# Optimization experiments

Hardware: AMD Instinct MI355X
Metric: run time of the kernel (lower is better)

The kernel has to match this reference:

```python
import math
import jax, jax.numpy as jnp
import numpy as np

B, N, C = 2, 2048, 1024
H = 16
D = C // H  # 64
LN_EPS = 1e-5


def setup_inputs() -> dict:
    key = jax.random.key(0)
    ks = jax.random.split(key, 5)
    x = jax.random.normal(ks[0], (B, N, C), dtype=jnp.float32)
    w_qkv = jax.random.normal(ks[1], (C, 3 * C), dtype=jnp.float32) * 0.02
    w_proj = jax.random.normal(ks[2], (C, C), dtype=jnp.float32) * 0.02
    b_proj = jnp.zeros((C,), dtype=jnp.float32)
    ln_w = jnp.ones((D,), dtype=jnp.float32) + jax.random.normal(ks[3], (D,), dtype=jnp.float32) * 0.02
    ln_b = jax.random.normal(ks[4], (D,), dtype=jnp.float32) * 0.02
    return {"x": x, "w_qkv": w_qkv, "w_proj": w_proj, "b_proj": b_proj,
            "ln_w": ln_w, "ln_b": ln_b}


def _layernorm(t, w, b):
    mu = jnp.mean(t, axis=-1, keepdims=True)
    var = jnp.var(t, axis=-1, keepdims=True)
    return (t - mu) * jax.lax.rsqrt(var + LN_EPS) * w + b


def reference(x, w_qkv, w_proj, b_proj, ln_w, ln_b):
    b, n, c = x.shape
    h, d = H, c // H
    # QKV projection (no bias): [b,n,3c] -> [3,b,h,n,d]
    qkv = (x @ w_qkv).reshape(b, n, 3, h, d).transpose(2, 0, 3, 1, 4)
    q, k, v = qkv[0], qkv[1], qkv[2]
    # per-head LayerNorm on q and k (qk_norm)
    q = _layernorm(q, ln_w, ln_b)
    k = _layernorm(k, ln_w, ln_b)
    # NOTE: source multiplies q by sqrt(head_dim) (faithful to original)
    q = q * jnp.asarray(math.sqrt(d), dtype=q.dtype)
    scores = jnp.einsum('bhnd,bhmd->bhnm', q, k)  # [b,h,n,n]
    mask_value = -jnp.finfo(scores.dtype).max
    causal = jnp.tril(jnp.ones((n, n), dtype=bool))
    scores = jnp.where(causal, scores, mask_value)
    attn = jax.nn.softmax(scores, axis=-1)
    out = jnp.einsum('bhnm,bhmd->bhnd', attn, v)  # [b,h,n,d]
    out = out.transpose(0, 2, 1, 3).reshape(b, n, c)  # b n (h d)
    return out @ w_proj + b_proj
```

## Files before the change

kernel.cpp:

```cpp
#include <hip/hip_runtime.h>

#define LOG2E 1.4426950408889634f

typedef _Float16 f16x8_t __attribute__((ext_vector_type(8)));
typedef _Float16 f16x4_t __attribute__((ext_vector_type(4)));
typedef float    f32x4_t __attribute__((ext_vector_type(4)));

#define MFMA32(a, b, c) __builtin_amdgcn_mfma_f32_16x16x32_f16(a, b, c, 0, 0, 0)
#define MFMA16(a, b, c) __builtin_amdgcn_mfma_f32_16x16x16f16(a, b, c, 0, 0, 0)

__device__ __forceinline__ void async_copy16(void* lds, const void* g) {
    __builtin_amdgcn_global_load_lds(
        (const __attribute__((address_space(1))) unsigned char*)g,
        (__attribute__((address_space(3))) unsigned char*)lds, 16, 0, 0);
}

__global__ void cast_f32_f16_k(const float* __restrict__ in, _Float16* __restrict__ out, int n4) {
    int i = blockIdx.x * blockDim.x + threadIdx.x;
    if (i >= n4) return;
    float4 v = ((const float4*)in)[i];
    f16x4_t o = { (_Float16)v.x, (_Float16)v.y, (_Float16)v.z, (_Float16)v.w };
    ((f16x4_t*)out)[i] = o;
}

__global__ void transpose_cast_k(const float* __restrict__ in, _Float16* __restrict__ out,
                                 int R, int C) {
    __shared__ _Float16 tl[64][65];
    const int t = threadIdx.x;
    const int c = t & 63;
    const int r4 = t >> 6;
    const int r0 = blockIdx.y * 64, c0 = blockIdx.x * 64;
#pragma unroll
    for (int i = 0; i < 16; ++i) {
        int r = r4 + i * 4;
        tl[c][r] = (_Float16)in[(size_t)(r0 + r) * C + c0 + c];
    }
    __syncthreads();
#pragma unroll
    for (int i = 0; i < 16; ++i) {
        int rr = r4 + i * 4;
        out[(size_t)(c0 + rr) * R + r0 + c] = tl[rr][c];
    }
}

__global__ void vtrans_k(const _Float16* __restrict__ qkv, _Float16* __restrict__ VTg) {
    __shared__ _Float16 tl[64][65];
    const int t = threadIdx.x;
    const int bh = blockIdx.x;
    const int b = bh >> 4, h = bh & 15;
    const int n0 = blockIdx.y * 64;
    const int c = t & 63;
    const int r4 = t >> 6;
#pragma unroll
    for (int i = 0; i < 16; ++i) {
        int r = r4 + i * 4;
        tl[c][r] = qkv[(size_t)(b * 2048 + n0 + r) * 3072 + 2048 + h * 64 + c];
    }
    __syncthreads();
#pragma unroll
    for (int i = 0; i < 16; ++i) {
        int d = r4 + i * 4;
        VTg[(size_t)bh * 131072 + (size_t)d * 2048 + n0 + c] = tl[d][c];
    }
}

template <typename OutT, bool BIAS>
__global__ __launch_bounds__(256, 2)
void gemm_f16_k(const _Float16* __restrict__ A, const _Float16* __restrict__ BT,
                OutT* __restrict__ C, const float* __restrict__ bias,
                int M, int N, int K) {
    __shared__ _Float16 As[2][128][32];
    __shared__ _Float16 Bs[2][128][32];
    const int tid = threadIdx.x;
    const int wid = tid >> 6, lane = tid & 63;
    const int qd = lane >> 4, ln = lane & 15;
    const int m0 = blockIdx.x * 128, n0 = blockIdx.y * 128;
    const int wm = (wid >> 1) * 64, wn = (wid & 1) * 64;

    f32x4_t acc[4][4] = {};

    const int srow = lane >> 2;
    const int skk  = (lane & 3) * 8;

    for (int k0 = 0; k0 < K; k0 += 64) {
        __syncthreads();
#pragma unroll
        for (int p = 0; p < 4; ++p) {
            const int seg = p * 4 + wid;
            const int s   = seg >> 3;
            const int rg  = seg & 7;
            const int row = rg * 16 + srow;
            const size_t goff = (size_t)row * K + k0 + s * 32 + skk;
            async_copy16(&As[0][0][0] + seg * 512, A  + (size_t)m0 * K + goff);
            async_copy16(&Bs[0][0][0] + seg * 512, BT + (size_t)n0 * K + goff);
        }
        __syncthreads();
#pragma unroll
        for (int s = 0; s < 2; ++s) {
            f16x8_t a[4], b[4];
#pragma unroll
            for (int i = 0; i < 4; ++i)
                a[i] = *(const f16x8_t*)&As[s][wm + i * 16 + ln][qd * 8];
#pragma unroll
            for (int j = 0; j < 4; ++j)
                b[j] = *(const f16x8_t*)&Bs[s][wn + j * 16 + ln][qd * 8];
#pragma unroll
            for (int i = 0; i < 4; ++i)
#pragma unroll
                for (int j = 0; j < 4; ++j)
                    acc[i][j] = MFMA32(a[i], b[j], acc[i][j]);
        }
    }
#pragma unroll
    for (int i = 0; i < 4; ++i)
#pragma unroll
        for (int j = 0; j < 4; ++j) {
            const int col = n0 + wn + j * 16 + ln;
            const float bv = BIAS ? bias[col] : 0.0f;
#pragma unroll
            for (int r = 0; r < 4; ++r) {
                const int row = m0 + wm + i * 16 + qd * 4 + r;
                C[(size_t)row * N + col] = (OutT)(acc[i][j][r] + bv);
            }
        }
}

__global__ __launch_bounds__(256, 2)
void gemm_f16_m64_k(const _Float16* __restrict__ A, const _Float16* __restrict__ BT,
                    float* __restrict__ C, const float* __restrict__ bias,
                    int M, int N, int K) {
    __shared__ _Float16 As[2][64][32];
    __shared__ _Float16 Bs[2][128][32];
    const int tid = threadIdx.x;
    const int wid = tid >> 6, lane = tid & 63;
    const int qd = lane >> 4, ln = lane & 15;
    const int m0 = blockIdx.x * 64, n0 = blockIdx.y * 128;
    const int wn = wid * 32;

    f32x4_t acc[4][2] = {};
    const int srow = lane >> 2;
    const int skk  = (lane & 3) * 8;

    for (int k0 = 0; k0 < K; k0 += 64) {
        __syncthreads();
#pragma unroll
        for (int p = 0; p < 2; ++p) {
            const int seg = p * 4 + wid;
            const int hidx = seg * 512 + lane * 8;
            const int s_ = hidx >> 11;
            const int row = (hidx >> 5) & 63;
            const int kk = hidx & 31;
            async_copy16(&As[0][0][0] + seg * 512,
                         A + (size_t)(m0 + row) * K + k0 + s_ * 32 + kk);
        }
#pragma unroll
        for (int p = 0; p < 4; ++p) {
            const int seg = p * 4 + wid;
            const int s   = seg >> 3;
            const int rg  = seg & 7;
            const int row = rg * 16 + srow;
            async_copy16(&Bs[0][0][0] + seg * 512,
                         BT + (size_t)(n0 + row) * K + k0 + s * 32 + skk);
        }
        __syncthreads();
#pragma unroll
        for (int s = 0; s < 2; ++s) {
            f16x8_t a[4], b[2];
#pragma unroll
            for (int i = 0; i < 4; ++i)
                a[i] = *(const f16x8_t*)&As[s][i * 16 + ln][qd * 8];
#pragma unroll
            for (int j = 0; j < 2; ++j)
                b[j] = *(const f16x8_t*)&Bs[s][wn + j * 16 + ln][qd * 8];
#pragma unroll
            for (int i = 0; i < 4; ++i)
#pragma unroll
                for (int j = 0; j < 2; ++j)
                    acc[i][j] = MFMA32(a[i], b[j], acc[i][j]);
        }
    }
#pragma unroll
    for (int i = 0; i < 4; ++i)
#pragma unroll
        for (int j = 0; j < 2; ++j) {
            const int col = n0 + wn + j * 16 + ln;
            const float bv = bias[col];
#pragma unroll
            for (int r = 0; r < 4; ++r) {
                const int row = m0 + i * 16 + qd * 4 + r;
                C[(size_t)row * N + col] = acc[i][j][r] + bv;
            }
        }
}

__global__ void ln_qk_k(const _Float16* __restrict__ qkv, const float* __restrict__ ln_w,
                        const float* __restrict__ ln_b, _Float16* __restrict__ Qb,
                        _Float16* __restrict__ Kb) {
    const int tid = threadIdx.x;
    const int wid = tid >> 6, lane = tid & 63;
    const int row = blockIdx.x * 4 + wid;
    const int t = row >> 4;
    const int h = row & 15;
    const int b = t >> 11, n = t & 2047;
    const size_t base = (size_t)t * 3072 + h * 64 + lane;
    float q = (float)qkv[base];
    float k = (float)qkv[base + 1024];
    const float wv = ln_w[lane], bv = ln_b[lane];

    float sq = q, sk = k;
#pragma unroll
    for (int m = 1; m < 64; m <<= 1) { sq += __shfl_xor(sq, m); sk += __shfl_xor(sk, m); }
    sq *= (1.0f / 64.0f); sk *= (1.0f / 64.0f);
    const float dq = q - sq, dk = k - sk;
    float vq = dq * dq, vk = dk * dk;
#pragma unroll
    for (int m = 1; m < 64; m <<= 1) { vq += __shfl_xor(vq, m); vk += __shfl_xor(vk, m); }
    vq *= (1.0f / 64.0f); vk *= (1.0f / 64.0f);
    const float yq = dq * rsqrtf(vq + 1e-5f) * wv + bv;
    const float yk = dk * rsqrtf(vk + 1e-5f) * wv + bv;
    const size_t obase = ((size_t)((b * 16 + h) * 2048 + n)) * 64 + lane;
    Qb[obase] = (_Float16)(yq * (8.0f * LOG2E));
    Kb[obase] = (_Float16)yk;
}

__global__ __launch_bounds__(128, 3)
void attn_k(const _Float16* __restrict__ Q, const _Float16* __restrict__ K,
            const _Float16* __restrict__ VTg, _Float16* __restrict__ O) {
    __shared__ _Float16 Ks[2][64][32];
    __shared__ _Float16 VT[64][64];

    const int tid = threadIdx.x;
    const int wid = tid >> 6, lane = tid & 63;
    const int qd = lane >> 4, ln = lane & 15;
    const int bh = blockIdx.x;
    const int b = bh >> 4, h = bh & 15;
    const int pr = blockIdx.y >> 1;
    const int half = blockIdx.y & 1;
    const int hib = 31 - pr, lob = pr;
    const size_t kvbase = (size_t)bh * 2048 * 64;
    const size_t vtbase = (size_t)bh * 131072;
    const int qh0 = hib * 64 + half * 32 + wid * 16;
    const int ql0 = lob * 64 + half * 32 + wid * 16;

    f16x8_t qfh[2], qfl[2];
#pragma unroll
    for (int s = 0; s < 2; ++s) {
        qfh[s] = *(const f16x8_t*)&Q[kvbase + (size_t)(qh0 + ln) * 64 + s * 32 + qd * 8];
        qfl[s] = *(const f16x8_t*)&Q[kvbase + (size_t)(ql0 + ln) * 64 + s * 32 + qd * 8];
    }

    f32x4_t oh[4] = {}, olo[4] = {};
    float mh = -3.0e38f, ml = -3.0e38f;
    float lh = 0.0f, ll = 0.0f;

    const int vrow = (lane >> 3);
    const int vY   = (lane & 7) ^ (vrow & 7);

    const int nst = hib + 1;

    for (int st = 0; st < nst; ++st) {
        const int kv0 = st * 64;
        __syncthreads();
#pragma unroll
        for (int p = 0; p < 4; ++p) {
            const int seg = p * 2 + wid;
            const int oh_ = seg * 512;
            const int hidx = oh_ + lane * 8;
            const int s_ = hidx >> 11;
            const int rrow = (hidx >> 5) & 63;
            const int kk = hidx & 31;
            async_copy16((_Float16*)Ks + oh_,
                         K + kvbase + (size_t)(kv0 + rrow) * 64 + s_ * 32 + kk);
        }
#pragma unroll
        for (int p = 0; p < 4; ++p) {
            const int seg = p * 2 + wid;
            const int d = seg * 8 + vrow;
            async_copy16(&VT[0][0] + seg * 512,
                         VTg + vtbase + (size_t)d * 2048 + kv0 + vY * 8);
        }
        __syncthreads();

        f16x8_t kb[4][2];
#pragma unroll
        for (int jt = 0; jt < 4; ++jt)
#pragma unroll
            for (int s = 0; s < 2; ++s)
                kb[jt][s] = *(const f16x8_t*)&Ks[s][jt * 16 + ln][qd * 8];
        f16x4_t vf[4][4];
#pragma unroll
        for (int dt = 0; dt < 4; ++dt)
#pragma unroll
            for (int c = 0; c < 4; ++c)
                vf[dt][c] = *(const f16x4_t*)
                    &VT[dt * 16 + ln][(((2 * c + (qd >> 1)) ^ (ln & 7)) << 3) + (qd & 1) * 4];

        auto process = [&](const f16x8_t (&qf)[2], f32x4_t (&o)[4], float& m, float& l,
                           int q0w, bool diag) {
            f32x4_t sc[4];
#pragma unroll
            for (int jt = 0; jt < 4; ++jt) {
                f32x4_t s = {};
                s = MFMA32(kb[jt][0], qf[0], s);
                s = MFMA32(kb[jt][1], qf[1], s);
                sc[jt] = s;
            }
            if (diag) {
                const int qq = q0w + ln;
#pragma unroll
                for (int c = 0; c < 4; ++c)
#pragma unroll
                    for (int r = 0; r < 4; ++r)
                        if (kv0 + c * 16 + qd * 4 + r > qq) sc[c][r] = -3.0e38f;
            }
            float mx = sc[0][0];
#pragma unroll
            for (int c = 0; c < 4; ++c)
#pragma unroll
                for (int r = 0; r < 4; ++r) mx = fmaxf(mx, sc[c][r]);
            mx = fmaxf(mx, __shfl_xor(mx, 16));
            mx = fmaxf(mx, __shfl_xor(mx, 32));
            const float mn = fmaxf(m, mx);
            const float al = exp2f(m - mn);
            m = mn;
            float rs = 0.0f;
            f16x4_t pf[4];
#pragma unroll
            for (int c = 0; c < 4; ++c)
#pragma unroll
                for (int r = 0; r < 4; ++r) {
                    const float p = exp2f(sc[c][r] - mn);
                    rs += p;
                    pf[c][r] = (_Float16)p;
                }
            l = l * al + rs;
#pragma unroll
            for (int dt = 0; dt < 4; ++dt) o[dt] *= al;
#pragma unroll
            for (int dt = 0; dt < 4; ++dt)
#pragma unroll
                for (int c = 0; c < 4; ++c)
                    o[dt] = MFMA16(vf[dt][c], pf[c], o[dt]);
        };

        process(qfh, oh, mh, lh, qh0, st == hib);
        if (st <= lob) process(qfl, olo, ml, ll, ql0, st == lob);
    }

    auto epi = [&](f32x4_t (&o)[4], float l, int q0w) {
        float t = l + __shfl_xor(l, 16);
        t = t + __shfl_xor(t, 32);
        const float inv = 1.0f / t;
        const size_t base = ((size_t)(b * 2048 + q0w + ln)) * 1024 + h * 64 + qd * 4;
#pragma unroll
        for (int dt = 0; dt < 4; ++dt) {
            f16x4_t ov;
#pragma unroll
            for (int r = 0; r < 4; ++r) ov[r] = (_Float16)(o[dt][r] * inv);
            *(f16x4_t*)&O[base + dt * 16] = ov;
        }
    };
    epi(oh, lh, qh0);
    epi(olo, ll, ql0);
}

extern "C" void kernel_launch(void* const* d_in, const int* in_sizes, int n_in,
                              void* d_out, int out_size, void* d_ws, size_t ws_size,
                              hipStream_t stream) {
    const float* x      = (const float*)d_in[0];
    const float* w_qkv  = (const float*)d_in[1];
    const float* w_proj = (const float*)d_in[2];
    const float* b_proj = (const float*)d_in[3];
    const float* ln_w   = (const float*)d_in[4];
    const float* ln_b   = (const float*)d_in[5];
    float* out = (float*)d_out;

    char* w = (char*)d_ws;
    _Float16*  qkv    = (_Float16*)w;  w += (size_t)4096 * 3072 * 2;
    _Float16*  xh     = (_Float16*)w;  w += (size_t)4096 * 1024 * 2;
    _Float16*  wqkvT  = (_Float16*)w;  w += (size_t)3072 * 1024 * 2;
    _Float16*  wprojT = (_Float16*)w;  w += (size_t)1024 * 1024 * 2;
    _Float16*  Qb     = (_Float16*)w;  w += (size_t)32 * 2048 * 64 * 2;
    _Float16*  Kb     = (_Float16*)w;  w += (size_t)32 * 2048 * 64 * 2;
    _Float16*  VTg    = (_Float16*)w;  w += (size_t)32 * 64 * 2048 * 2;
    _Float16*  Ah     = (_Float16*)w;  w += (size_t)4096 * 1024 * 2;

    cast_f32_f16_k<<<4096, 256, 0, stream>>>(x, xh, 4096 * 1024 / 4);
    transpose_cast_k<<<dim3(48, 16), 256, 0, stream>>>(w_qkv, wqkvT, 1024, 3072);
    transpose_cast_k<<<dim3(16, 16), 256, 0, stream>>>(w_proj, wprojT, 1024, 1024);
    gemm_f16_k<_Float16, false><<<dim3(32, 24), 256, 0, stream>>>(xh, wqkvT, qkv, nullptr, 4096, 3072, 1024);
    vtrans_k<<<dim3(32, 32), 256, 0, stream>>>(qkv, VTg);
    ln_qk_k<<<16384, 256, 0, stream>>>(qkv, ln_w, ln_b, Qb, Kb);
    attn_k<<<dim3(32, 32), 128, 0, stream>>>(Qb, Kb, VTg, Ah);
    gemm_f16_m64_k<<<dim3(64, 8), 256, 0, stream>>>(Ah, wprojT, out, b_proj, 4096, 1024, 1024);
}
```

Measured before the change: 234.1 us.

## Split causal attention into KV chunks with double-buffered staging and merge pass

```diff
diff --git a/kernel.cpp b/kernel.cpp
--- a/kernel.cpp
+++ b/kernel.cpp
@@ -223,135 +223,134 @@
     Kb[obase] = (_Float16)yk;
 }
 
-__global__ __launch_bounds__(128, 3)
-void attn_k(const _Float16* __restrict__ Q, const _Float16* __restrict__ K,
-            const _Float16* __restrict__ VTg, _Float16* __restrict__ O) {
-    __shared__ _Float16 Ks[2][64][32];
-    __shared__ _Float16 VT[64][64];
+__global__ __launch_bounds__(256, 3)
+void attn_part_k(const _Float16* __restrict__ Q, const _Float16* __restrict__ K,
+                 const _Float16* __restrict__ VTg, _Float16* __restrict__ O,
+                 float* __restrict__ Op, float* __restrict__ ml) {
+    __shared__ _Float16 Ks[2][2][64][32];
+    __shared__ _Float16 VT[2][64][64];
 
     const int tid = threadIdx.x;
     const int wid = tid >> 6, lane = tid & 63;
     const int qd = lane >> 4, ln = lane & 15;
     const int bh = blockIdx.x;
     const int b = bh >> 4, h = bh & 15;
-    const int pr = blockIdx.y >> 1;
-    const int half = blockIdx.y & 1;
-    const int hib = 31 - pr, lob = pr;
+    const int y = blockIdx.y;
+    int band, chunk, nst;
+    if (y < 16)      { band = 16 + y; chunk = 0; nst = 16; }
+    else if (y < 32) { band = 47 - y; chunk = 1; nst = band - 15; }
+    else             { band = 47 - y; chunk = 0; nst = band + 1; }
     const size_t kvbase = (size_t)bh * 2048 * 64;
     const size_t vtbase = (size_t)bh * 131072;
-    const int qh0 = hib * 64 + half * 32 + wid * 16;
-    const int ql0 = lob * 64 + half * 32 + wid * 16;
-
-    f16x8_t qfh[2], qfl[2];
-#pragma unroll
-    for (int s = 0; s < 2; ++s) {
-        qfh[s] = *(const f16x8_t*)&Q[kvbase + (size_t)(qh0 + ln) * 64 + s * 32 + qd * 8];
-        qfl[s] = *(const f16x8_t*)&Q[kvbase + (size_t)(ql0 + ln) * 64 + s * 32 + qd * 8];
-    }
-
-    f32x4_t oh[4] = {}, olo[4] = {};
-    float mh = -3.0e38f, ml = -3.0e38f;
-    float lh = 0.0f, ll = 0.0f;
-
-    const int vrow = (lane >> 3);
+    const int qrow0 = band * 64 + wid * 16;
+    const int kvbeg = chunk * 1024;
+
+    f16x8_t qf[2];
+#pragma unroll
+    for (int s = 0; s < 2; ++s)
+        qf[s] = *(const f16x8_t*)&Q[kvbase + (size_t)(qrow0 + ln) * 64 + s * 32 + qd * 8];
+
+    f32x4_t o[4] = {};
+    float m = -3.0e38f, l = 0.0f;
+
+    const int vrow = lane >> 3;
     const int vY   = (lane & 7) ^ (vrow & 7);
-
-    const int nst = hib + 1;
-
-    for (int st = 0; st < nst; ++st) {
-        const int kv0 = st * 64;
-        __syncthreads();
-#pragma unroll
-        for (int p = 0; p < 4; ++p) {
-            const int seg = p * 2 + wid;
-            const int oh_ = seg * 512;
-            const int hidx = oh_ + lane * 8;
+    const int khidx_base = lane * 8;
+
+    auto stage = [&](int buf, int kv0) {
+#pragma unroll
+        for (int p = 0; p < 2; ++p) {
+            const int seg = p * 4 + wid;
+            const int hidx = seg * 512 + khidx_base;
             const int s_ = hidx >> 11;
             const int rrow = (hidx >> 5) & 63;
             const int kk = hidx & 31;
-            async_copy16((_Float16*)Ks + oh_,
+            async_copy16(&Ks[buf][0][0][0] + seg * 512,
                          K + kvbase + (size_t)(kv0 + rrow) * 64 + s_ * 32 + kk);
         }
 #pragma unroll
-        for (int p = 0; p < 4; ++p) {
-            const int seg = p * 2 + wid;
+        for (int p = 0; p < 2; ++p) {
+            const int seg = p * 4 + wid;
             const int d = seg * 8 + vrow;
-            async_copy16(&VT[0][0] + seg * 512,
+            async_copy16(&VT[buf][0][0] + seg * 512,
                          VTg + vtbase + (size_t)d * 2048 + kv0 + vY * 8);
         }
+    };
+
+    stage(0, kvbeg);
+
+    for (int st = 0; st < nst; ++st) {
+        const int kv0 = kvbeg + st * 64;
         __syncthreads();
+        if (st + 1 < nst) stage((st + 1) & 1, kv0 + 64);
+        const int buf = st & 1;
 
         f16x8_t kb[4][2];
 #pragma unroll
         for (int jt = 0; jt < 4; ++jt)
 #pragma unroll
             for (int s = 0; s < 2; ++s)
-                kb[jt][s] = *(const f16x8_t*)&Ks[s][jt * 16 + ln][qd * 8];
+                kb[jt][s] = *(const f16x8_t*)&Ks[buf][s][jt * 16 + ln][qd * 8];
         f16x4_t vf[4][4];
 #pragma unroll
         for (int dt = 0; dt < 4; ++dt)
 #pragma unroll
             for (int c = 0; c < 4; ++c)
                 vf[dt][c] = *(const f16x4_t*)
-                    &VT[dt * 16 + ln][(((2 * c + (qd >> 1)) ^ (ln & 7)) << 3) + (qd & 1) * 4];
-
-        auto process = [&](const f16x8_t (&qf)[2], f32x4_t (&o)[4], float& m, float& l,
-                           int q0w, bool diag) {
-            f32x4_t sc[4];
-#pragma unroll
-            for (int jt = 0; jt < 4; ++jt) {
-                f32x4_t s = {};
-                s = MFMA32(kb[jt][0], qf[0], s);
-                s = MFMA32(kb[jt][1], qf[1], s);
-                sc[jt] = s;
+                    &VT[buf][dt * 16 + ln][(((2 * c + (qd >> 1)) ^ (ln & 7)) << 3) + (qd & 1) * 4];
+
+        f32x4_t sc[4];
+#pragma unroll
+        for (int jt = 0; jt < 4; ++jt) {
+            f32x4_t s = {};
+            s = MFMA32(kb[jt][0], qf[0], s);
+            s = MFMA32(kb[jt][1], qf[1], s);
+            sc[jt] = s;
+        }
+        if (chunk * 16 + st == band) {
+            const int qq = qrow0 + ln;
+#pragma unroll
+            for (int c = 0; c < 4; ++c)
+#pragma unroll
+                for (int r = 0; r < 4; ++r)
+                    if (kv0 + c * 16 + qd * 4 + r > qq) sc[c][r] = -3.0e38f;
+        }
+        float mx = sc[0][0];
+#pragma unroll
+        for (int c = 0; c < 4; ++c)
+#pragma unroll
+            for (int r = 0; r < 4; ++r) mx = fmaxf(mx, sc[c][r]);
+        mx = fmaxf(mx, __shfl_xor(mx, 16));
+        mx = fmaxf(mx, __shfl_xor(mx, 32));
+        const float mn = fmaxf(m, mx);
+        const float al = exp2f(m - mn);
+        m = mn;
+        float rs = 0.0f;
+        f16x4_t pf[4];
+#pragma unroll
+        for (int c = 0; c < 4; ++c)
+#pragma unroll
+            for (int r = 0; r < 4; ++r) {
+                const float p = exp2f(sc[c][r] - mn);
+                rs += p;
+                pf[c][r] = (_Float16)p;
             }
-            if (diag) {
-                const int qq = q0w + ln;
-#pragma unroll
-                for (int c = 0; c < 4; ++c)
-#pragma unroll
-                    for (int r = 0; r < 4; ++r)
-                        if (kv0 + c * 16 + qd * 4 + r > qq) sc[c][r] = -3.0e38f;
-            }
-            float mx = sc[0][0];
+        l = l * al + rs;
+#pragma unroll
+        for (int dt = 0; dt < 4; ++dt) o[dt] *= al;
+#pragma unroll
+        for (int dt = 0; dt < 4; ++dt)
 #pragma unroll
             for (int c = 0; c < 4; ++c)
-#pragma unroll
-                for (int r = 0; r < 4; ++r) mx = fmaxf(mx, sc[c][r]);
-            mx = fmaxf(mx, __shfl_xor(mx, 16));
-            mx = fmaxf(mx, __shfl_xor(mx, 32));
-            const float mn = fmaxf(m, mx);
-            const float al = exp2f(m - mn);
-            m = mn;
-            float rs = 0.0f;
-            f16x4_t pf[4];
-#pragma unroll
-            for (int c = 0; c < 4; ++c)
-#pragma unroll
-                for (int r = 0; r < 4; ++r) {
-                    const float p = exp2f(sc[c][r] - mn);
-                    rs += p;
-                    pf[c][r] = (_Float16)p;
-                }
-            l = l * al + rs;
-#pragma unroll
-            for (int dt = 0; dt < 4; ++dt) o[dt] *= al;
-#pragma unroll
-            for (int dt = 0; dt < 4; ++dt)
-#pragma unroll
-                for (int c = 0; c < 4; ++c)
-                    o[dt] = MFMA16(vf[dt][c], pf[c], o[dt]);
-        };
-
-        process(qfh, oh, mh, lh, qh0, st == hib);
-        if (st <= lob) process(qfl, olo, ml, ll, ql0, st == lob);
-    }
-
-    auto epi = [&](f32x4_t (&o)[4], float l, int q0w) {
-        float t = l + __shfl_xor(l, 16);
-        t = t + __shfl_xor(t, 32);
-        const float inv = 1.0f / t;
-        const size_t base = ((size_t)(b * 2048 + q0w + ln)) * 1024 + h * 64 + qd * 4;
+                o[dt] = MFMA16(vf[dt][c], pf[c], o[dt]);
+    }
+
+    float lt = l + __shfl_xor(l, 16);
+    lt = lt + __shfl_xor(lt, 32);
+
+    if (band < 16) {
+        const float inv = 1.0f / lt;
+        const size_t base = ((size_t)(b * 2048 + qrow0 + ln)) * 1024 + h * 64 + qd * 4;
 #pragma unroll
         for (int dt = 0; dt < 4; ++dt) {
             f16x4_t ov;
@@ -359,9 +358,48 @@
             for (int r = 0; r < 4; ++r) ov[r] = (_Float16)(o[dt][r] * inv);
             *(f16x4_t*)&O[base + dt * 16] = ov;
         }
-    };
-    epi(oh, lh, qh0);
-    epi(olo, ll, ql0);
+    } else {
+        const size_t pb = (((size_t)bh * 16 + (band - 16)) * 2 + chunk);
+        const int row = wid * 16 + ln;
+        float* op = Op + pb * 4096 + (size_t)row * 64 + qd * 4;
+#pragma unroll
+        for (int dt = 0; dt < 4; ++dt)
+            *(f32x4_t*)&op[dt * 16] = o[dt];
+        if (qd == 0) {
+            ml[pb * 128 + row * 2]     = m;
+            ml[pb * 128 + row * 2 + 1] = lt;
+        }
+    }
+}
+
+__global__ __launch_bounds__(256)
+void attn_merge_k(const float* __restrict__ Op, const float* __restrict__ ml,
+                  _Float16* __restrict__ O) {
+    const int bh = blockIdx.x, bnd = blockIdx.y;
+    const int b = bh >> 4, h = bh & 15;
+    const int band = 16 + bnd;
+    const size_t pb = ((size_t)bh * 16 + bnd) * 2;
+    const int tid = threadIdx.x;
+    const int row = tid >> 2;
+    const int c4 = (tid & 3) * 16;
+    const float m0 = ml[pb * 128 + row * 2],     l0 = ml[pb * 128 + row * 2 + 1];
+    const float m1 = ml[pb * 128 + 128 + row * 2], l1 = ml[pb * 128 + 128 + row * 2 + 1];
+    const float mm = fmaxf(m0, m1);
+    const float a0 = exp2f(m0 - mm), a1 = exp2f(m1 - mm);
+    const float inv = 1.0f / (l0 * a0 + l1 * a1);
+    const float* p0 = Op + pb * 4096 + (size_t)row * 64 + c4;
+    const float* p1 = p0 + 4096;
+    _Float16* op = O + ((size_t)(b * 2048 + band * 64 + row)) * 1024 + h * 64 + c4;
+#pragma unroll
+    for (int g = 0; g < 4; ++g) {
+        f32x4_t v0 = *(const f32x4_t*)&p0[g * 4];
+        f32x4_t v1 = *(const f32x4_t*)&p1[g * 4];
+        f16x4_t ov;
+#pragma unroll
+        for (int r = 0; r < 4; ++r)
+            ov[r] = (_Float16)((v0[r] * a0 + v1[r] * a1) * inv);
+        *(f16x4_t*)&op[g * 4] = ov;
+    }
 }
 
 extern "C" void kernel_launch(void* const* d_in, const int* in_sizes, int n_in,
@@ -384,6 +422,8 @@
     _Float16*  Kb     = (_Float16*)w;  w += (size_t)32 * 2048 * 64 * 2;
     _Float16*  VTg    = (_Float16*)w;  w += (size_t)32 * 64 * 2048 * 2;
     _Float16*  Ah     = (_Float16*)w;  w += (size_t)4096 * 1024 * 2;
+    float*     Op     = (float*)w;     w += (size_t)32 * 16 * 2 * 4096 * 4;
+    float*     mlb    = (float*)w;     w += (size_t)32 * 16 * 2 * 128 * 4;
 
     cast_f32_f16_k<<<4096, 256, 0, stream>>>(x, xh, 4096 * 1024 / 4);
     transpose_cast_k<<<dim3(48, 16), 256, 0, stream>>>(w_qkv, wqkvT, 1024, 3072);
@@ -391,6 +431,7 @@
     gemm_f16_k<_Float16, false><<<dim3(32, 24), 256, 0, stream>>>(xh, wqkvT, qkv, nullptr, 4096, 3072, 1024);
     vtrans_k<<<dim3(32, 32), 256, 0, stream>>>(qkv, VTg);
     ln_qk_k<<<16384, 256, 0, stream>>>(qkv, ln_w, ln_b, Qb, Kb);
-    attn_k<<<dim3(32, 32), 128, 0, stream>>>(Qb, Kb, VTg, Ah);
+    attn_part_k<<<dim3(32, 48), 256, 0, stream>>>(Qb, Kb, VTg, Ah, Op, mlb);
+    attn_merge_k<<<dim3(32, 16), 256, 0, stream>>>(Op, mlb, Ah);
     gemm_f16_m64_k<<<dim3(64, 8), 256, 0, stream>>>(Ah, wprojT, out, b_proj, 4096, 1024, 1024);
 }
```

Result: faster. 210.0 us (-10.3%).
